# Optimization experiments

Hardware: AMD Instinct MI355X
Metric: run time of the kernel (lower is better)

Reference implementation:

```python
import jax, jax.numpy as jnp
import numpy as np

C_S, C_V, C_Z, C_OUT = 32, 8, 128, 128
IN_S, IN_V = 28, 37
N_RBF, N_POS = 64, 64
IN_Z = N_RBF * 25 + N_POS          # 1664 raw pairwise-dist RBF + positional feats
N_LAYERS, K = 4, 30
N_NODES = 1024
N_EDGES = N_NODES * K
WEIGHT_NUMEL = C_S*C_S + C_S*C_V + C_V*C_V + C_V*C_S + C_V*C_V  # 1664
LN_EPS = 1e-5
BN_EPS = 1e-5


def _ln(x, g, b):
    m = x.mean(-1, keepdims=True)
    v = x.var(-1, keepdims=True)
    return (x - m) / jnp.sqrt(v + LN_EPS) * g + b


def _tp(xs, xv, sh_s, sh_v, w):
    """FullyConnectedTensorProduct (32x0e+8x1e) x (0e+1e) -> (32x0e+8x1e), per-edge weights w [E, WEIGHT_NUMEL]."""
    E = w.shape[0]
    o = [0]
    def cut(n1, n2):
        ww = w[:, o[0]:o[0] + n1 * n2].reshape(E, n1, n2)
        o[0] += n1 * n2
        return ww
    w1 = cut(C_S, C_S)  # 0e x 0e -> 0e
    w2 = cut(C_S, C_V)  # 0e x 1e -> 1e
    w3 = cut(C_V, C_V)  # 1e x 0e -> 1e
    w4 = cut(C_V, C_S)  # 1e x 1e -> 0e (dot)
    w5 = cut(C_V, C_V)  # 1e x 1e -> 1e (cross)
    # path normalization: 1/sqrt(in1_mul * n_paths_to_output)
    a1 = 1.0 / np.sqrt(2 * C_S)
    a4 = 1.0 / np.sqrt(2 * C_V)
    a2 = 1.0 / np.sqrt(3 * C_S)
    a3 = 1.0 / np.sqrt(3 * C_V)
    a5 = a3
    out_s = a1 * jnp.einsum('e,ei,eij->ej', sh_s, xs, w1) \
          + (a4 / np.sqrt(3.0)) * jnp.einsum('eix,ex,eij->ej', xv, sh_v, w4)
    cross = jnp.cross(xv, sh_v[:, None, :])  # [E, C_V, 3]
    out_v = a2 * jnp.einsum('ei,eij,ex->ejx', xs, w2, sh_v) \
          + a3 * jnp.einsum('e,eix,eij->ejx', sh_s, xv, w3) \
          + (a5 / np.sqrt(2.0)) * jnp.einsum('eix,eij->ejx', cross, w5)
    return out_s, out_v


def _forward(node_raw, edge_raw, edge_vecs, rot,
             ee_w1, ee_b1, ee_w2, ee_b2, ee_w3, ee_b3, ee_ln_g, ee_ln_b,
             ne_ws, ne_wv,
             fc_w1, fc_b1, fc_w2, fc_b2, bn_g, bn_b, bn_vg,
             eu_lin, eu_w1, eu_b1, eu_w2, eu_b2, eu_w3, eu_b3, eu_ln_g, eu_ln_b,
             mu_w, mu_b, lv_w, lv_b, edge_index):
    N = node_raw.shape[0]
    dst, src = edge_index[0], edge_index[1]
    # spherical harmonics, lmax=1, 'component' normalization: Y0 = 1, Y1 = sqrt(3) * unit
    unit = edge_vecs / (jnp.linalg.norm(edge_vecs, axis=-1, keepdims=True) + 1e-8)
    sh_s = jnp.ones(edge_vecs.shape[0], node_raw.dtype)
    sh_v = np.sqrt(3.0) * unit
    # edge embed MLP + LN
    h = jax.nn.relu(edge_raw @ ee_w1 + ee_b1)
    h = jax.nn.relu(h @ ee_w2 + ee_b2)
    ef = _ln(h @ ee_w3 + ee_b3, ee_ln_g, ee_ln_b)
    # node embed: per-irrep (equivariant) linear 28x0e->32x0e, 37x1e->8x1e
    xs = node_raw[:, :IN_S] @ ne_ws
    xv = jnp.einsum('nix,ij->njx', node_raw[:, IN_S:].reshape(N, IN_V, 3), ne_wv)
    cnt = jnp.maximum(jax.ops.segment_sum(jnp.ones_like(src, node_raw.dtype), src, num_segments=N), 1.0)
    for l in range(N_LAYERS):
        # per-edge TP weights from edge features
        w = jax.nn.relu(ef @ fc_w1[l] + fc_b1[l]) @ fc_w2[l] + fc_b2[l]  # [E, WEIGHT_NUMEL]
        ms, mv = _tp(xs[dst], xv[dst], sh_s, sh_v, w)
        ags = jax.ops.segment_sum(ms, src, num_segments=N) / cnt[:, None]
        agv = jax.ops.segment_sum(mv, src, num_segments=N) / cnt[:, None, None]
        xs = xs + ags  # pad is a no-op: in/out irreps identical
        xv = xv + agv
        # e3nn-style BatchNorm (batch statistics)
        xs = (xs - xs.mean(0)) / jnp.sqrt(xs.var(0) + BN_EPS) * bn_g[l] + bn_b[l]
        fn = jnp.mean(jnp.sum(xv ** 2, -1), 0) / 3.0  # per-channel mean component norm
        xv = xv / jnp.sqrt(fn + BN_EPS)[None, :, None] * bn_vg[l][None, :, None]
        # EdgeUpdate
        a = xs @ eu_lin[l]  # scalar part -> h_edge
        e_in = jnp.concatenate([a[dst], a[src], ef], -1)
        u = jax.nn.relu(e_in @ eu_w1[l] + eu_b1[l])
        u = jax.nn.relu(u @ eu_w2[l] + eu_b2[l])
        u = u @ eu_w3[l] + eu_b3[l]
        ef = _ln(ef + u, eu_ln_g[l], eu_ln_b[l])
    # scalarize vectors w.r.t. per-node frames: R^T v
    xv_loc = jnp.einsum('nxy,ncx->ncy', rot, xv)
    feat = jnp.concatenate([xs, xv_loc.reshape(N, -1)], -1)  # [N, 56]
    mu = feat @ mu_w + mu_b
    lv = feat @ lv_w + lv_b
    return jnp.stack([mu, lv])  # [2, N, C_OUT]


def setup_inputs() -> dict:
    key = jax.random.key(0)
    ks = iter(jax.random.split(key, 80))
    def nrm(shape, fan=None):
        s = 1.0 if fan is None else 1.0 / np.sqrt(fan)
        return jax.random.normal(next(ks), shape, jnp.float32) * s
    inp = {}
    inp['node_raw'] = nrm([N_NODES, IN_S + 3 * IN_V])
    inp['edge_raw'] = nrm([N_EDGES, IN_Z])
    inp['edge_vecs'] = nrm([N_EDGES, 3])
    inp['rot'] = jnp.linalg.qr(nrm([N_NODES, 3, 3]))[0]
    inp['edge_index'] = jax.random.randint(next(ks), (2, N_EDGES), 0, N_NODES, jnp.int32)
    inp['ee_w1'] = nrm([IN_Z, C_Z], IN_Z); inp['ee_b1'] = jnp.zeros([C_Z])
    inp['ee_w2'] = nrm([C_Z, C_Z], C_Z);   inp['ee_b2'] = jnp.zeros([C_Z])
    inp['ee_w3'] = nrm([C_Z, C_Z], C_Z);   inp['ee_b3'] = jnp.zeros([C_Z])
    inp['ee_ln_g'] = jnp.ones([C_Z]); inp['ee_ln_b'] = jnp.zeros([C_Z])
    inp['ne_ws'] = nrm([IN_S, C_S], IN_S)
    inp['ne_wv'] = nrm([IN_V, C_V], IN_V)
    L = N_LAYERS
    inp['fc_w1'] = nrm([L, C_Z, C_Z], C_Z); inp['fc_b1'] = jnp.zeros([L, C_Z])
    inp['fc_w2'] = nrm([L, C_Z, WEIGHT_NUMEL], C_Z); inp['fc_b2'] = jnp.zeros([L, WEIGHT_NUMEL])
    inp['bn_g'] = jnp.ones([L, C_S]); inp['bn_b'] = jnp.zeros([L, C_S]); inp['bn_vg'] = jnp.ones([L, C_V])
    inp['eu_lin'] = nrm([L, C_S, C_Z], C_S)
    inp['eu_w1'] = nrm([L, 3 * C_Z, C_Z], 3 * C_Z); inp['eu_b1'] = jnp.zeros([L, C_Z])
    inp['eu_w2'] = nrm([L, C_Z, C_Z], C_Z); inp['eu_b2'] = jnp.zeros([L, C_Z])
    inp['eu_w3'] = nrm([L, C_Z, C_Z], C_Z); inp['eu_b3'] = jnp.zeros([L, C_Z])
    inp['eu_ln_g'] = jnp.ones([L, C_Z]); inp['eu_ln_b'] = jnp.zeros([L, C_Z])
    D = C_S + 3 * C_V
    inp['mu_w'] = nrm([D, C_OUT], D); inp['mu_b'] = jnp.zeros([C_OUT])
    inp['lv_w'] = nrm([D, C_OUT], D); inp['lv_b'] = jnp.zeros([C_OUT])
    return inp


def reference(node_raw, edge_raw, edge_vecs, rot,
              ee_w1, ee_b1, ee_w2, ee_b2, ee_w3, ee_b3, ee_ln_g, ee_ln_b,
              ne_ws, ne_wv,
              fc_w1, fc_b1, fc_w2, fc_b2, bn_g, bn_b, bn_vg,
              eu_lin, eu_w1, eu_b1, eu_w2, eu_b2, eu_w3, eu_b3, eu_ln_g, eu_ln_b,
              mu_w, mu_b, lv_w, lv_b, edge_index):
    return _forward(node_raw, edge_raw, edge_vecs, rot,
                    ee_w1, ee_b1, ee_w2, ee_b2, ee_w3, ee_b3, ee_ln_g, ee_ln_b,
                    ne_ws, ne_wv,
                    fc_w1, fc_b1, fc_w2, fc_b2, bn_g, bn_b, bn_vg,
                    eu_lin, eu_w1, eu_b1, eu_w2, eu_b2, eu_w3, eu_b3, eu_ln_g, eu_ln_b,
                    mu_w, mu_b, lv_w, lv_b, edge_index)
```

## Files before the change

### kernel.cpp

```cpp
#include <hip/hip_runtime.h>
#include <hip/hip_bf16.h>

typedef __hip_bfloat16 bf16;
typedef __attribute__((ext_vector_type(8))) short s16x8;
typedef __attribute__((ext_vector_type(4))) float f32x4;

#define NN 1024
#define NE 30720
#define CS 32
#define CV 8
#define CZ 128
#define INS 28
#define INV 37
#define NRDIM 139
#define INZ 1664
#define WN 1664
#define NL 4

__device__ __forceinline__ float b2f(bf16 x) { return __bfloat162float(x); }
__device__ __forceinline__ bf16 f2b(float x) { return __float2bfloat16(x); }


template<int RELU, int AF32, int GATHER>
__global__ __launch_bounds__(256)
void gemm64(const void* __restrict__ Ap, const bf16* __restrict__ Bf,
            const float* __restrict__ bias, bf16* __restrict__ Cp,
            int M, int K,
            const bf16* __restrict__ g_a, const bf16* __restrict__ g_ef,
            const int* __restrict__ g_ei)
{
    __shared__ __align__(16) bf16 la[64 * 40];
    const int bm = blockIdx.x * 64;
    const int tid = threadIdx.x;
    const int lane = tid & 63;
    const int wv = tid >> 6;
    const int lr = tid >> 1;
    const int lc = (tid & 1) * 16;
    const int l15 = lane & 15;
    const int quad = lane >> 4;
    const int K32 = K >> 5;
    f32x4 acc[4][2] = {};
    const bf16*  ga16 = (const bf16*) Ap + (size_t)(bm + lr) * K + lc;
    const float* ga32 = (const float*)Ap + (size_t)(bm + lr) * K + lc;
    int gdst = 0, gsrc = 0, grow = 0;
    if (GATHER && tid < 128) {
        grow = bm + lr;
        gdst = g_ei[grow];
        gsrc = g_ei[NE + grow];
    }
    for (int k0 = 0; k0 < K; k0 += 32) {
        union { bf16 h[16]; float4 q[2]; } pa;
        if (tid < 128) {
            if (AF32) {
                float4 f0 = *(const float4*)(ga32 + k0);
                float4 f1 = *(const float4*)(ga32 + k0 + 4);
                float4 f2 = *(const float4*)(ga32 + k0 + 8);
                float4 f3 = *(const float4*)(ga32 + k0 + 12);
                pa.h[0]=f2b(f0.x); pa.h[1]=f2b(f0.y); pa.h[2]=f2b(f0.z); pa.h[3]=f2b(f0.w);
                pa.h[4]=f2b(f1.x); pa.h[5]=f2b(f1.y); pa.h[6]=f2b(f1.z); pa.h[7]=f2b(f1.w);
                pa.h[8]=f2b(f2.x); pa.h[9]=f2b(f2.y); pa.h[10]=f2b(f2.z); pa.h[11]=f2b(f2.w);
                pa.h[12]=f2b(f3.x); pa.h[13]=f2b(f3.y); pa.h[14]=f2b(f3.z); pa.h[15]=f2b(f3.w);
            } else if (GATHER) {
                int kk = k0 + lc;
                const bf16* src;
                if (kk < 128)      src = g_a  + (size_t)gdst * CZ + kk;
                else if (kk < 256) src = g_a  + (size_t)gsrc * CZ + (kk - 128);
                else               src = g_ef + (size_t)grow * CZ + (kk - 256);
                pa.q[0] = *(const float4*)src;
                pa.q[1] = *(const float4*)(src + 8);
            } else {
                pa.q[0] = *(const float4*)(ga16 + k0);
                pa.q[1] = *(const float4*)(ga16 + k0 + 8);
            }
        }
        s16x8 bfr[2];
#pragma unroll
        for (int ni = 0; ni < 2; ni++)
            bfr[ni] = *(const s16x8*)(Bf + (size_t)(((wv * 2 + ni) * K32 + (k0 >> 5)) * 512) + lane * 8);
        __syncthreads();
        if (tid < 128) {
            *(float4*)&la[lr * 40 + lc]     = pa.q[0];
            *(float4*)&la[lr * 40 + lc + 8] = pa.q[1];
        }
        __syncthreads();
        s16x8 af[4];
#pragma unroll
        for (int mi = 0; mi < 4; mi++)
            af[mi] = *(const s16x8*)&la[(mi * 16 + l15) * 40 + quad * 8];
#pragma unroll
        for (int mi = 0; mi < 4; mi++)
#pragma unroll
            for (int ni = 0; ni < 2; ni++)
                acc[mi][ni] = __builtin_amdgcn_mfma_f32_16x16x32_bf16(af[mi], bfr[ni], acc[mi][ni], 0, 0, 0);
    }
#pragma unroll
    for (int ni = 0; ni < 2; ni++) {
        const int col = wv * 32 + ni * 16 + l15;
        const float bv = bias[col];
#pragma unroll
        for (int mi = 0; mi < 4; mi++) {
            const int row0 = bm + mi * 16 + quad * 4;
#pragma unroll
            for (int r = 0; r < 4; r++) {
                float v = acc[mi][ni][r] + bv;
                if (RELU) v = fmaxf(v, 0.f);
                Cp[(size_t)(row0 + r) * CZ + col] = f2b(v);
            }
        }
    }
}

template<int RESID>
__global__ __launch_bounds__(256)
void mlp2(const bf16* __restrict__ A,
          const bf16* __restrict__ w2f, const float* __restrict__ b2,
          const bf16* __restrict__ w3f, const float* __restrict__ b3,
          const float* __restrict__ g, const float* __restrict__ bb,
          bf16* efb)
{
    __shared__ __align__(16) bf16 s_a[64 * 136];
    __shared__ __align__(16) bf16 s_u[64 * 136];
    __shared__ float s_o[64 * 132];
    const int bm = blockIdx.x * 64;
    const int t = threadIdx.x;
    const int lane = t & 63;
    const int wv = t >> 6;
    const int l15 = lane & 15;
    const int quad = lane >> 4;
    {
        int r = t >> 2, c0 = (t & 3) * 32;
        const float4* s4 = (const float4*)(A + (size_t)(bm + r) * CZ + c0);
        float4* d4 = (float4*)&s_a[r * 136 + c0];
        d4[0] = s4[0]; d4[1] = s4[1]; d4[2] = s4[2]; d4[3] = s4[3];
    }
    __syncthreads();
    s16x8 af[4][4];
#pragma unroll
    for (int mi = 0; mi < 4; mi++)
#pragma unroll
        for (int kk = 0; kk < 4; kk++)
            af[mi][kk] = *(const s16x8*)&s_a[(mi * 16 + l15) * 136 + kk * 32 + quad * 8];
#pragma unroll
    for (int s = 0; s < 2; s++) {
        int n = wv * 32 + s * 16 + l15;
        f32x4 acc[4] = {};
#pragma unroll
        for (int kk = 0; kk < 4; kk++) {
            s16x8 bfr = *(const s16x8*)(w2f + (size_t)(((wv * 2 + s) * 4 + kk) * 512) + lane * 8);
#pragma unroll
            for (int mi = 0; mi < 4; mi++)
                acc[mi] = __builtin_amdgcn_mfma_f32_16x16x32_bf16(af[mi][kk], bfr, acc[mi], 0, 0, 0);
        }
        float bv = b2[n];
#pragma unroll
        for (int mi = 0; mi < 4; mi++)
#pragma unroll
            for (int r = 0; r < 4; r++)
                s_u[(mi * 16 + quad * 4 + r) * 136 + n] = f2b(fmaxf(acc[mi][r] + bv, 0.f));
    }
    __syncthreads();
#pragma unroll
    for (int mi = 0; mi < 4; mi++)
#pragma unroll
        for (int kk = 0; kk < 4; kk++)
            af[mi][kk] = *(const s16x8*)&s_u[(mi * 16 + l15) * 136 + kk * 32 + quad * 8];
#pragma unroll
    for (int s = 0; s < 2; s++) {
        int n = wv * 32 + s * 16 + l15;
        f32x4 acc[4] = {};
#pragma unroll
        for (int kk = 0; kk < 4; kk++) {
            s16x8 bfr = *(const s16x8*)(w3f + (size_t)(((wv * 2 + s) * 4 + kk) * 512) + lane * 8);
#pragma unroll
            for (int mi = 0; mi < 4; mi++)
                acc[mi] = __builtin_amdgcn_mfma_f32_16x16x32_bf16(af[mi][kk], bfr, acc[mi], 0, 0, 0);
        }
        float bv = b3[n];
#pragma unroll
        for (int mi = 0; mi < 4; mi++)
#pragma unroll
            for (int r = 0; r < 4; r++)
                s_o[(mi * 16 + quad * 4 + r) * 132 + n] = acc[mi][r] + bv;
    }
    __syncthreads();
    {
        int row = wv * 16 + (lane >> 2);
        int q = lane & 3;
        int col0 = q * 32;
        size_t gbase = (size_t)(bm + row) * CZ;
        float s = 0.f, s2 = 0.f;
        for (int i = 0; i < 32; i++) {
            float x = s_o[row * 132 + col0 + i];
            if (RESID) x += b2f(efb[gbase + col0 + i]);
            s += x; s2 += x * x;
        }
        s  += __shfl_xor(s, 1);  s2 += __shfl_xor(s2, 1);
        s  += __shfl_xor(s, 2);  s2 += __shfl_xor(s2, 2);
        float mean = s * (1.f / 128.f);
        float var  = s2 * (1.f / 128.f) - mean * mean;
        float rstd = rsqrtf(var + 1e-5f);
        for (int i = 0; i < 32; i++) {
            int col = col0 + i;
            float x = s_o[row * 132 + col];
            if (RESID) x += b2f(efb[gbase + col]);
            efb[gbase + col] = f2b((x - mean) * rstd * g[col] + bb[col]);
        }
    }
}

__global__ __launch_bounds__(256, 2)
void fc2_tp(const bf16* __restrict__ ef,
            const bf16* __restrict__ w1f, const float* __restrict__ b1,
            const bf16* __restrict__ w2f, const float* __restrict__ b2,
            const int* __restrict__ ei, const float* __restrict__ edge_vecs,
            const float* __restrict__ xs, const float* __restrict__ xv,
            float* __restrict__ tp_s, float* __restrict__ tp_v)
{
    __shared__ __align__(16) bf16 s_a[64 * 136];
    __shared__ __align__(16) bf16 s_h[64 * 136];
    __shared__ __align__(16) float s_xsT[32][64];
    __shared__ __align__(16) float s_xvT[24][64];
    __shared__ __align__(16) float s_crT[24][64];
    __shared__ __align__(16) float s_y4T[8][64];
    __shared__ __align__(16) float s_b2[WN];
    __shared__ float s_shv[64][3];
    __shared__ int s_dst[64];
    __shared__ float s_os[64][32];
    __shared__ float s_ov[64][24];
    const int be = blockIdx.x * 64;
    const int t = threadIdx.x;
    const int lane = t & 63;
    const int wv = t >> 6;
    const int l15 = lane & 15;
    const int quad = lane >> 4;
    const int q4 = quad * 4;

    if (t < 64) {
        int e = be + t;
        s_dst[t] = ei[e];
        float vx = edge_vecs[e * 3 + 0];
        float vy = edge_vecs[e * 3 + 1];
        float vz = edge_vecs[e * 3 + 2];
        float sc = 1.7320508075688772f / (sqrtf(vx * vx + vy * vy + vz * vz) + 1e-8f);
        s_shv[t][0] = vx * sc; s_shv[t][1] = vy * sc; s_shv[t][2] = vz * sc;
    }
    for (int i = t; i < 64 * 32; i += 256) ((float*)s_os)[i] = 0.f;
    for (int i = t; i < 64 * 24; i += 256) ((float*)s_ov)[i] = 0.f;
    for (int i = t; i < WN; i += 256) s_b2[i] = b2[i];
    {
        int r = t >> 2, c0 = (t & 3) * 32;
        const float4* s4 = (const float4*)(ef + (size_t)(be + r) * CZ + c0);
        float4* d4 = (float4*)&s_a[r * 136 + c0];
        d4[0] = s4[0]; d4[1] = s4[1]; d4[2] = s4[2]; d4[3] = s4[3];
    }
    __syncthreads();
    for (int i = t; i < 64 * 32; i += 256) { int e = i & 63, c = i >> 6; s_xsT[c][e] = xs[s_dst[e] * CS + c]; }
    for (int i = t; i < 64 * 24; i += 256) { int e = i & 63, c = i >> 6; s_xvT[c][e] = xv[s_dst[e] * 24 + c]; }
    __syncthreads();
    for (int i2 = t; i2 < 512; i2 += 256) {
        int e = i2 & 63, i = i2 >> 6;
        float h0 = s_shv[e][0], h1 = s_shv[e][1], h2 = s_shv[e][2];
        float x0 = s_xvT[i * 3 + 0][e], x1 = s_xvT[i * 3 + 1][e], x2 = s_xvT[i * 3 + 2][e];
        s_y4T[i][e] = 1.1547005383792515f * (x0 * h0 + x1 * h1 + x2 * h2);
        s_crT[i * 3 + 0][e] = 0.7071067811865476f * (x1 * h2 - x2 * h1);
        s_crT[i * 3 + 1][e] = 0.7071067811865476f * (x2 * h0 - x0 * h2);
        s_crT[i * 3 + 2][e] = 0.7071067811865476f * (x0 * h1 - x1 * h0);
    }
    {
        s16x8 af1[4][4];
#pragma unroll
        for (int mi = 0; mi < 4; mi++)
#pragma unroll
            for (int kk = 0; kk < 4; kk++)
                af1[mi][kk] = *(const s16x8*)&s_a[(mi * 16 + l15) * 136 + kk * 32 + quad * 8];
#pragma unroll
        for (int s = 0; s < 2; s++) {
            int n = wv * 32 + s * 16 + l15;
            f32x4 acc[4] = {};
#pragma unroll
            for (int kk = 0; kk < 4; kk++) {
                s16x8 bfr = *(const s16x8*)(w1f + (size_t)(((wv * 2 + s) * 4 + kk) * 512) + lane * 8);
#pragma unroll
                for (int mi = 0; mi < 4; mi++)
                    acc[mi] = __builtin_amdgcn_mfma_f32_16x16x32_bf16(af1[mi][kk], bfr, acc[mi], 0, 0, 0);
            }
            float bv = b1[n];
#pragma unroll
            for (int mi = 0; mi < 4; mi++)
#pragma unroll
                for (int r = 0; r < 4; r++)
                    s_h[(mi * 16 + quad * 4 + r) * 136 + n] = f2b(fmaxf(acc[mi][r] + bv, 0.f));
        }
    }
    __syncthreads();
    s16x8 af[4][4];
#pragma unroll
    for (int mi = 0; mi < 4; mi++)
#pragma unroll
        for (int kk = 0; kk < 4; kk++)
            af[mi][kk] = *(const s16x8*)&s_h[(mi * 16 + l15) * 136 + kk * 32 + quad * 8];
    float os[4][4] = {}, sv2[4][4] = {}, ov0[4][4] = {}, ov1[4][4] = {}, ov2[4][4] = {};
    const int ib = l15 >> 3;
    for (int nt = wv; nt < 104; nt += 4) {
        const float bv = s_b2[nt * 16 + l15];
        const bf16* wb = w2f + (size_t)(nt * 4) * 512 + lane * 8;
        s16x8 bfr[4];
#pragma unroll
        for (int kk = 0; kk < 4; kk++)
            bfr[kk] = *(const s16x8*)(wb + kk * 512);
        f32x4 ac[4] = {};
#pragma unroll
        for (int kk = 0; kk < 4; kk++)
#pragma unroll
            for (int mi = 0; mi < 4; mi++)
                ac[mi] = __builtin_amdgcn_mfma_f32_16x16x32_bf16(af[mi][kk], bfr[kk], ac[mi], 0, 0, 0);
        if (nt < 64) {
            const int i = nt >> 1;
#pragma unroll
            for (int mi = 0; mi < 4; mi++) {
                float4 f = *(const float4*)&s_xsT[i][mi * 16 + q4];
                os[mi][0] += (ac[mi][0] + bv) * f.x; os[mi][1] += (ac[mi][1] + bv) * f.y;
                os[mi][2] += (ac[mi][2] + bv) * f.z; os[mi][3] += (ac[mi][3] + bv) * f.w;
            }
        } else if (nt < 80) {
            const int i = (nt - 64) * 2 + ib;
#pragma unroll
            for (int mi = 0; mi < 4; mi++) {
                float4 f = *(const float4*)&s_xsT[i][mi * 16 + q4];
                sv2[mi][0] += (ac[mi][0] + bv) * f.x; sv2[mi][1] += (ac[mi][1] + bv) * f.y;
                sv2[mi][2] += (ac[mi][2] + bv) * f.z; sv2[mi][3] += (ac[mi][3] + bv) * f.w;
            }
        } else if (nt < 84) {
            const int i0 = ((nt - 80) * 2 + ib) * 3;
#pragma unroll
            for (int mi = 0; mi < 4; mi++) {
                float4 f0 = *(const float4*)&s_xvT[i0 + 0][mi * 16 + q4];
                float4 f1 = *(const float4*)&s_xvT[i0 + 1][mi * 16 + q4];
                float4 f2 = *(const float4*)&s_xvT[i0 + 2][mi * 16 + q4];
                float w0 = ac[mi][0] + bv, w1 = ac[mi][1] + bv, w2 = ac[mi][2] + bv, w3 = ac[mi][3] + bv;
                ov0[mi][0] += w0 * f0.x; ov0[mi][1] += w1 * f0.y; ov0[mi][2] += w2 * f0.z; ov0[mi][3] += w3 * f0.w;
                ov1[mi][0] += w0 * f1.x; ov1[mi][1] += w1 * f1.y; ov1[mi][2] += w2 * f1.z; ov1[mi][3] += w3 * f1.w;
                ov2[mi][0] += w0 * f2.x; ov2[mi][1] += w1 * f2.y; ov2[mi][2] += w2 * f2.z; ov2[mi][3] += w3 * f2.w;
            }
        } else if (nt < 100) {
            const int i = (nt - 84) >> 1;
#pragma unroll
            for (int mi = 0; mi < 4; mi++) {
                float4 f = *(const float4*)&s_y4T[i][mi * 16 + q4];
                os[mi][0] += (ac[mi][0] + bv) * f.x; os[mi][1] += (ac[mi][1] + bv) * f.y;
                os[mi][2] += (ac[mi][2] + bv) * f.z; os[mi][3] += (ac[mi][3] + bv) * f.w;
            }
        } else {
            const int i0 = ((nt - 100) * 2 + ib) * 3;
#pragma unroll
            for (int mi = 0; mi < 4; mi++) {
                float4 f0 = *(const float4*)&s_crT[i0 + 0][mi * 16 + q4];
                float4 f1 = *(const float4*)&s_crT[i0 + 1][mi * 16 + q4];
                float4 f2 = *(const float4*)&s_crT[i0 + 2][mi * 16 + q4];
                float w0 = ac[mi][0] + bv, w1 = ac[mi][1] + bv, w2 = ac[mi][2] + bv, w3 = ac[mi][3] + bv;
                ov0[mi][0] += w0 * f0.x; ov0[mi][1] += w1 * f0.y; ov0[mi][2] += w2 * f0.z; ov0[mi][3] += w3 * f0.w;
                ov1[mi][0] += w0 * f1.x; ov1[mi][1] += w1 * f1.y; ov1[mi][2] += w2 * f1.z; ov1[mi][3] += w3 * f1.w;
                ov2[mi][0] += w0 * f2.x; ov2[mi][1] += w1 * f2.y; ov2[mi][2] += w2 * f2.z; ov2[mi][3] += w3 * f2.w;
            }
        }
    }
    {
        const int jo = (wv & 1) * 16 + l15;
        const int jv3 = (l15 & 7) * 3;
#pragma unroll
        for (int mi = 0; mi < 4; mi++)
#pragma unroll
            for (int r = 0; r < 4; r++) {
                int e = mi * 16 + quad * 4 + r;
                atomicAdd(&s_os[e][jo], os[mi][r]);
                float sv = 0.5f * sv2[mi][r];
                atomicAdd(&s_ov[e][jv3 + 0], ov0[mi][r] + s_shv[e][0] * sv);
                atomicAdd(&s_ov[e][jv3 + 1], ov1[mi][r] + s_shv[e][1] * sv);
                atomicAdd(&s_ov[e][jv3 + 2], ov2[mi][r] + s_shv[e][2] * sv);
            }
    }
    __syncthreads();
    for (int i = t; i < 64 * 32; i += 256) {
        int e = i >> 5, d = i & 31;
        tp_s[(size_t)(be + e) * 32 + d] = s_os[e][d] * 0.125f;
    }
    for (int i = t; i < 64 * 24; i += 256) {
        int e = i / 24, d = i - e * 24;
        tp_v[(size_t)(be + e) * 24 + d] = s_ov[e][d] * 0.2041241452319315f;
    }
}

__global__ __launch_bounds__(1024)
void scan_csr(const int* __restrict__ cnt, int* __restrict__ row_start,
              int* __restrict__ fillpos, float* __restrict__ icnt)
{
    __shared__ int tmp[1024];
    int t = threadIdx.x;
    int v = cnt[t];
    tmp[t] = v;
    __syncthreads();
    for (int o = 1; o < 1024; o <<= 1) {
        int x = (t >= o) ? tmp[t - o] : 0;
        __syncthreads();
        tmp[t] += x;
        __syncthreads();
    }
    int excl = tmp[t] - v;
    row_start[t] = excl;
    fillpos[t] = excl;
    if (t == 1023) row_start[1024] = tmp[1023];
    icnt[t] = 1.0f / (float)(v > 1 ? v : 1);
}

__global__ void fill_perm(const int* __restrict__ ei, int* __restrict__ fillpos,
                          int* __restrict__ perm)
{
    int e = blockIdx.x * 256 + threadIdx.x;
    if (e < NE) {
        int s = ei[NE + e];
        int p = atomicAdd(&fillpos[s], 1);
        perm[p] = e;
    }
}

__global__ __launch_bounds__(64)
void aggregate(const float* __restrict__ tp_s, const float* __restrict__ tp_v,
               const int* __restrict__ perm, const int* __restrict__ row_start,
               const float* __restrict__ icnt,
               float* __restrict__ ags, float* __restrict__ agv)
{
    __shared__ int s_e[64];
    const int n = blockIdx.x, t = threadIdx.x;
    const int s = row_start[n], epe = row_start[n + 1];
    float acc = 0.f;
    for (int k0 = s; k0 < epe; k0 += 64) {
        int kk = k0 + t;
        s_e[t] = (kk < epe) ? perm[kk] : 0;
        __syncthreads();
        int m = epe - k0; if (m > 64) m = 64;
        for (int j = 0; j < m; j++) {
            int e = s_e[j];
            acc += (t < 32) ? tp_s[(size_t)e * 32 + t]
                            : tp_v[(size_t)e * 24 + (t - 32)];
        }
        __syncthreads();
    }
    acc *= icnt[n];
    if (t < 32) ags[n * CS + t] = acc;
    else if (t < 56) agv[n * 24 + (t - 32)] = acc;
}

__device__ __forceinline__ void fragseg(int i, int R, int C,
                                        const float* __restrict__ s, bf16* __restrict__ d)
{
    int l = i / (R * C);
    int rem = i - l * R * C;
    int k = rem / C;
    int n = rem - k * C;
    int dst = ((n >> 4) * (R >> 5) + (k >> 5)) * 512 + ((k >> 3) & 3) * 128 + (n & 15) * 8 + (k & 7);
    d[(size_t)l * R * C + dst] = f2b(s[i]);
}

__global__ void transpose_all(const float* __restrict__ p0, const float* __restrict__ p1,
                              const float* __restrict__ p2, const float* __restrict__ p3,
                              const float* __restrict__ p4, const float* __restrict__ p5,
                              const float* __restrict__ p6, const float* __restrict__ p7,
                              bf16* d0, bf16* d1, bf16* d2, bf16* d3,
                              bf16* d4, bf16* d5, bf16* d6, bf16* d7)
{
    int i = blockIdx.x * 256 + threadIdx.x;
    const int S0 = INZ * CZ;
    const int S1 = CZ * CZ;
    const int S2 = CZ * CZ;
    const int S3 = NL * CZ * CZ;
    const int S4 = NL * CZ * WN;
    const int S5 = NL * 384 * CZ;
    const int S6 = NL * CZ * CZ;
    const int S7 = NL * CZ * CZ;
    if (i < S0) { fragseg(i, INZ, CZ, p0, d0); return; } i -= S0;
    if (i < S1) { fragseg(i, CZ, CZ, p1, d1); return; }  i -= S1;
    if (i < S2) { fragseg(i, CZ, CZ, p2, d2); return; }  i -= S2;
    if (i < S3) { fragseg(i, CZ, CZ, p3, d3); return; }  i -= S3;
    if (i < S4) { fragseg(i, CZ, WN, p4, d4); return; }  i -= S4;
    if (i < S5) { fragseg(i, 384, CZ, p5, d5); return; } i -= S5;
    if (i < S6) { fragseg(i, CZ, CZ, p6, d6); return; }  i -= S6;
    if (i < S7) { fragseg(i, CZ, CZ, p7, d7); return; }
}

__global__ __launch_bounds__(64)
void node_embed(const float* __restrict__ node_raw, const float* __restrict__ ne_ws,
                const float* __restrict__ ne_wv, float* __restrict__ xs, float* __restrict__ xv)
{
    int n = blockIdx.x, t = threadIdx.x;
    const float* nr = node_raw + (size_t)n * NRDIM;
    if (t < 32) {
        float acc = 0.f;
        for (int i = 0; i < INS; i++) acc += nr[i] * ne_ws[i * CS + t];
        xs[n * CS + t] = acc;
    } else if (t < 56) {
        int t2 = t - 32, j = t2 / 3, x = t2 - 3 * (t2 / 3);
        float acc = 0.f;
        for (int i = 0; i < INV; i++) acc += nr[INS + i * 3 + x] * ne_wv[i * CV + j];
        xv[n * 24 + t2] = acc;
    }
}

__global__ void count_src(const int* __restrict__ ei, int* __restrict__ cnt)
{
    int e = blockIdx.x * 256 + threadIdx.x;
    if (e < NE) atomicAdd(&cnt[ei[NE + e]], 1);
}

__global__ __launch_bounds__(256)
void bnfused(float* __restrict__ xs, float* __restrict__ xv,
             const float* __restrict__ ags, const float* __restrict__ agv,
             const float* __restrict__ g, const float* __restrict__ b,
             const float* __restrict__ vg)
{
    __shared__ float red[8];
    __shared__ float stat[2];
    int c = blockIdx.x, t = threadIdx.x;
    if (c < 32) {
        float s = 0.f, s2 = 0.f;
        for (int n = t; n < NN; n += 256) {
            float v = xs[n * CS + c] + ags[n * CS + c];
            s += v; s2 += v * v;
        }
        for (int o = 32; o > 0; o >>= 1) { s += __shfl_down(s, o); s2 += __shfl_down(s2, o); }
        int w = t >> 6;
        if ((t & 63) == 0) { red[w * 2] = s; red[w * 2 + 1] = s2; }
        __syncthreads();
        if (t == 0) {
            float S = red[0] + red[2] + red[4] + red[6];
            float S2 = red[1] + red[3] + red[5] + red[7];
            float mean = S * (1.f / NN);
            float var = S2 * (1.f / NN) - mean * mean;
            stat[0] = mean;
            stat[1] = rsqrtf(var + 1e-5f);
        }
        __syncthreads();
        float mean = stat[0], rstd = stat[1], gg = g[c], bb = b[c];
        for (int n = t; n < NN; n += 256) {
            int ix = n * CS + c;
            float v = xs[ix] + ags[ix];
            xs[ix] = (v - mean) * rstd * gg + bb;
        }
    } else {
        int c2 = c - 32;
        float s = 0.f;
        for (int n = t; n < NN; n += 256) {
            float v0 = xv[n * 24 + c2 * 3 + 0] + agv[n * 24 + c2 * 3 + 0];
            float v1 = xv[n * 24 + c2 * 3 + 1] + agv[n * 24 + c2 * 3 + 1];
            float v2 = xv[n * 24 + c2 * 3 + 2] + agv[n * 24 + c2 * 3 + 2];
            s += v0 * v0 + v1 * v1 + v2 * v2;
        }
        for (int o = 32; o > 0; o >>= 1) s += __shfl_down(s, o);
        int w = t >> 6;
        if ((t & 63) == 0) red[w] = s;
        __syncthreads();
        if (t == 0) {
            float fn = (red[0] + red[1] + red[2] + red[3]) * (1.f / (3.f * NN));
            stat[0] = vg[c2] * rsqrtf(fn + 1e-5f);
        }
        __syncthreads();
        float scale = stat[0];
        for (int n = t; n < NN; n += 256) {
            for (int x = 0; x < 3; x++) {
                int ix = n * 24 + c2 * 3 + x;
                xv[ix] = (xv[ix] + agv[ix]) * scale;
            }
        }
    }
}

__global__ __launch_bounds__(128)
void lin_a(const float* __restrict__ xs, const float* __restrict__ eu_lin_l,
           bf16* __restrict__ a_b)
{
    __shared__ float sxs[32];
    int n = blockIdx.x, t = threadIdx.x;
    if (t < 32) sxs[t] = xs[n * CS + t];
    __syncthreads();
    float acc = 0.f;
    for (int c = 0; c < 32; c++) acc += sxs[c] * eu_lin_l[c * CZ + t];
    a_b[(size_t)n * CZ + t] = f2b(acc);
}

__global__ __launch_bounds__(128)
void final_out(const float* __restrict__ xs, const float* __restrict__ xv,
               const float* __restrict__ rot,
               const float* __restrict__ mu_w, const float* __restrict__ mu_b,
               const float* __restrict__ lv_w, const float* __restrict__ lv_b,
               float* __restrict__ out)
{
    __shared__ float feat[56];
    int n = blockIdx.x, t = threadIdx.x;
    if (t < 32) feat[t] = xs[n * CS + t];
    else if (t < 56) {
        int t2 = t - 32, c = t2 / 3, y = t2 - 3 * (t2 / 3);
        float acc = 0.f;
        for (int x = 0; x < 3; x++)
            acc += rot[n * 9 + x * 3 + y] * xv[n * 24 + c * 3 + x];
        feat[t] = acc;
    }
    __syncthreads();
    float mu = mu_b[t], lv = lv_b[t];
    for (int d = 0; d < 56; d++) {
        float f = feat[d];
        mu += f * mu_w[d * 128 + t];
        lv += f * lv_w[d * 128 + t];
    }
    out[(size_t)n * 128 + t] = mu;
    out[(size_t)NN * 128 + (size_t)n * 128 + t] = lv;
}

extern "C" void kernel_launch(void* const* d_in, const int* in_sizes, int n_in,
                              void* d_out, int out_size, void* d_ws, size_t ws_size,
                              hipStream_t stream)
{
    (void)in_sizes; (void)n_in; (void)out_size; (void)ws_size;
    const float* node_raw  = (const float*)d_in[0];
    const float* edge_raw  = (const float*)d_in[1];
    const float* edge_vecs = (const float*)d_in[2];
    const float* rot       = (const float*)d_in[3];
    const int*   ei        = (const int*  )d_in[4];
    const float* ee_w1 = (const float*)d_in[5];
    const float* ee_b1 = (const float*)d_in[6];
    const float* ee_w2 = (const float*)d_in[7];
    const float* ee_b2 = (const float*)d_in[8];
    const float* ee_w3 = (const float*)d_in[9];
    const float* ee_b3 = (const float*)d_in[10];
    const float* ee_ln_g = (const float*)d_in[11];
    const float* ee_ln_b = (const float*)d_in[12];
    const float* ne_ws = (const float*)d_in[13];
    const float* ne_wv = (const float*)d_in[14];
    const float* fc_w1 = (const float*)d_in[15];
    const float* fc_b1 = (const float*)d_in[16];
    const float* fc_w2 = (const float*)d_in[17];
    const float* fc_b2 = (const float*)d_in[18];
    const float* bn_g  = (const float*)d_in[19];
    const float* bn_b  = (const float*)d_in[20];
    const float* bn_vg = (const float*)d_in[21];
    const float* eu_lin = (const float*)d_in[22];
    const float* eu_w1 = (const float*)d_in[23];
    const float* eu_b1 = (const float*)d_in[24];
    const float* eu_w2 = (const float*)d_in[25];
    const float* eu_b2 = (const float*)d_in[26];
    const float* eu_w3 = (const float*)d_in[27];
    const float* eu_b3 = (const float*)d_in[28];
    const float* eu_ln_g = (const float*)d_in[29];
    const float* eu_ln_b = (const float*)d_in[30];
    const float* mu_w = (const float*)d_in[31];
    const float* mu_b = (const float*)d_in[32];
    const float* lv_w = (const float*)d_in[33];
    const float* lv_b = (const float*)d_in[34];

    char* ws = (char*)d_ws;
    size_t off = 0;
    auto alloc = [&](size_t bytes) -> void* {
        void* p = ws + off;
        off += (bytes + 255) & ~(size_t)255;
        return p;
    };
    bf16*  ef_b  = (bf16*) alloc((size_t)NE * CZ * 2);
    bf16*  buf_a = (bf16*) alloc((size_t)NE * CZ * 2);
    float* xs    = (float*)alloc((size_t)NN * CS * 4);
    float* xv    = (float*)alloc((size_t)NN * 24 * 4);
    float* ags   = (float*)alloc((size_t)NN * CS * 4);
    float* agv   = (float*)alloc((size_t)NN * 24 * 4);
    int*   cnti  = (int*)  alloc((size_t)NN * 4);
    float* icnt  = (float*)alloc((size_t)NN * 4);
    bf16*  a_b   = (bf16*) alloc((size_t)NN * CZ * 2);
    float* tp_s  = (float*)alloc((size_t)NE * 32 * 4);
    float* tp_v  = (float*)alloc((size_t)NE * 24 * 4 + 64);
    int*   perm  = (int*)  alloc((size_t)NE * 4);
    int*   row_start = (int*)alloc((size_t)(NN + 1) * 4);
    int*   fillpos   = (int*)alloc((size_t)NN * 4);
    bf16* ee_w1t = (bf16*)alloc((size_t)INZ * CZ * 2);
    bf16* ee_w2t = (bf16*)alloc((size_t)CZ * CZ * 2);
    bf16* ee_w3t = (bf16*)alloc((size_t)CZ * CZ * 2);
    bf16* fc_w1t = (bf16*)alloc((size_t)NL * CZ * CZ * 2);
    bf16* fc_w2t = (bf16*)alloc((size_t)NL * WN * CZ * 2);
    bf16* eu_w1t = (bf16*)alloc((size_t)NL * 384 * CZ * 2);
    bf16* eu_w2t = (bf16*)alloc((size_t)NL * CZ * CZ * 2);
    bf16* eu_w3t = (bf16*)alloc((size_t)NL * CZ * CZ * 2);

    const int TRN = INZ*CZ + 2*CZ*CZ + NL*CZ*CZ + NL*CZ*WN + NL*384*CZ + 2*NL*CZ*CZ;
    transpose_all<<<(TRN + 255) / 256, 256, 0, stream>>>(
        ee_w1, ee_w2, ee_w3, fc_w1, fc_w2, eu_w1, eu_w2, eu_w3,
        ee_w1t, ee_w2t, ee_w3t, fc_w1t, fc_w2t, eu_w1t, eu_w2t, eu_w3t);

    node_embed<<<NN, 64, 0, stream>>>(node_raw, ne_ws, ne_wv, xs, xv);
    hipMemsetAsync(cnti, 0, NN * 4, stream);
    count_src<<<NE / 256, 256, 0, stream>>>(ei, cnti);
    scan_csr<<<1, 1024, 0, stream>>>(cnti, row_start, fillpos, icnt);
    fill_perm<<<NE / 256, 256, 0, stream>>>(ei, fillpos, perm);

    const int GE = NE / 64;
    gemm64<1, 1, 0><<<GE, 256, 0, stream>>>(edge_raw, ee_w1t, ee_b1, buf_a, NE, INZ, nullptr, nullptr, nullptr);
    mlp2<0><<<GE, 256, 0, stream>>>(buf_a, ee_w2t, ee_b2, ee_w3t, ee_b3, ee_ln_g, ee_ln_b, ef_b);

    for (int l = 0; l < NL; l++) {
        fc2_tp<<<NE / 64, 256, 0, stream>>>(
            ef_b, fc_w1t + (size_t)l * CZ * CZ, fc_b1 + l * CZ,
            fc_w2t + (size_t)l * WN * CZ, fc_b2 + l * WN,
            ei, edge_vecs, xs, xv, tp_s, tp_v);
        aggregate<<<NN, 64, 0, stream>>>(tp_s, tp_v, perm, row_start, icnt, ags, agv);
        bnfused<<<40, 256, 0, stream>>>(xs, xv, ags, agv,
                                        bn_g + l * CS, bn_b + l * CS, bn_vg + l * CV);
        lin_a<<<NN, 128, 0, stream>>>(xs, eu_lin + (size_t)l * CS * CZ, a_b);
        gemm64<1, 0, 1><<<GE, 256, 0, stream>>>(
            nullptr, eu_w1t + (size_t)l * 384 * CZ, eu_b1 + l * CZ, buf_a, NE, 384, a_b, ef_b, ei);
        mlp2<1><<<GE, 256, 0, stream>>>(buf_a, eu_w2t + (size_t)l * CZ * CZ, eu_b2 + l * CZ,
                                        eu_w3t + (size_t)l * CZ * CZ, eu_b3 + l * CZ,
                                        eu_ln_g + l * CZ, eu_ln_b + l * CZ, ef_b);
    }

    final_out<<<NN, 128, 0, stream>>>(xs, xv, rot, mu_w, mu_b, lv_w, lv_b, (float*)d_out);
}
```

Measured before the change: 946.6 us.

## Fold node linear into edge-update W1 and fuse edge-update MLP into one kernel

Precomputes eu_lin·W1 products for the dst and src blocks so each node's contribution to the first edge-update layer is a per-node 128-wide vector, replacing a 384-K gathered GEMM with a 128-K GEMM plus a gathered add. The whole edge-update MLP (three layers, residual and layer norm) is fused into one kernel, so the intermediate activation no longer round-trips through global memory. In exchange it adds a small fold kernel, per-node fp32 projection buffers, and a change in rounding because the node terms are no longer quantized to bf16 before the matmul.

Measured after the change: 877.4 us. -7.3%, faster.

```diff
diff --git a/kernel.cpp b/kernel.cpp
--- a/kernel.cpp
+++ b/kernel.cpp
@@ -21,13 +21,11 @@
 __device__ __forceinline__ bf16 f2b(float x) { return __float2bfloat16(x); }
 
 
-template<int RELU, int AF32, int GATHER>
+template<int RELU, int AF32>
 __global__ __launch_bounds__(256)
 void gemm64(const void* __restrict__ Ap, const bf16* __restrict__ Bf,
             const float* __restrict__ bias, bf16* __restrict__ Cp,
-            int M, int K,
-            const bf16* __restrict__ g_a, const bf16* __restrict__ g_ef,
-            const int* __restrict__ g_ei)
+            int M, int K)
 {
     __shared__ __align__(16) bf16 la[64 * 40];
     const int bm = blockIdx.x * 64;
@@ -42,12 +40,6 @@
     f32x4 acc[4][2] = {};
     const bf16*  ga16 = (const bf16*) Ap + (size_t)(bm + lr) * K + lc;
     const float* ga32 = (const float*)Ap + (size_t)(bm + lr) * K + lc;
-    int gdst = 0, gsrc = 0, grow = 0;
-    if (GATHER && tid < 128) {
-        grow = bm + lr;
-        gdst = g_ei[grow];
-        gsrc = g_ei[NE + grow];
-    }
     for (int k0 = 0; k0 < K; k0 += 32) {
         union { bf16 h[16]; float4 q[2]; } pa;
         if (tid < 128) {
@@ -60,14 +52,6 @@
                 pa.h[4]=f2b(f1.x); pa.h[5]=f2b(f1.y); pa.h[6]=f2b(f1.z); pa.h[7]=f2b(f1.w);
                 pa.h[8]=f2b(f2.x); pa.h[9]=f2b(f2.y); pa.h[10]=f2b(f2.z); pa.h[11]=f2b(f2.w);
                 pa.h[12]=f2b(f3.x); pa.h[13]=f2b(f3.y); pa.h[14]=f2b(f3.z); pa.h[15]=f2b(f3.w);
-            } else if (GATHER) {
-                int kk = k0 + lc;
-                const bf16* src;
-                if (kk < 128)      src = g_a  + (size_t)gdst * CZ + kk;
-                else if (kk < 256) src = g_a  + (size_t)gsrc * CZ + (kk - 128);
-                else               src = g_ef + (size_t)grow * CZ + (kk - 256);
-                pa.q[0] = *(const float4*)src;
-                pa.q[1] = *(const float4*)(src + 8);
             } else {
                 pa.q[0] = *(const float4*)(ga16 + k0);
                 pa.q[1] = *(const float4*)(ga16 + k0 + 8);
@@ -110,7 +94,6 @@
     }
 }
 
-template<int RESID>
 __global__ __launch_bounds__(256)
 void mlp2(const bf16* __restrict__ A,
           const bf16* __restrict__ w2f, const float* __restrict__ b2,
@@ -191,7 +174,6 @@
         float s = 0.f, s2 = 0.f;
         for (int i = 0; i < 32; i++) {
             float x = s_o[row * 132 + col0 + i];
-            if (RESID) x += b2f(efb[gbase + col0 + i]);
             s += x; s2 += x * x;
         }
         s  += __shfl_xor(s, 1);  s2 += __shfl_xor(s2, 1);
@@ -202,7 +184,150 @@
         for (int i = 0; i < 32; i++) {
             int col = col0 + i;
             float x = s_o[row * 132 + col];
-            if (RESID) x += b2f(efb[gbase + col]);
+            efb[gbase + col] = f2b((x - mean) * rstd * g[col] + bb[col]);
+        }
+    }
+}
+
+__global__ __launch_bounds__(256)
+void eu_fused(bf16* __restrict__ efb,
+              const float* __restrict__ adg, const float* __restrict__ asg,
+              const int* __restrict__ ei,
+              const bf16* __restrict__ w1cf, const float* __restrict__ b1,
+              const bf16* __restrict__ w2f, const float* __restrict__ b2,
+              const bf16* __restrict__ w3f, const float* __restrict__ b3,
+              const float* __restrict__ g, const float* __restrict__ bb)
+{
+    __shared__ __align__(16) bf16 s_a[64 * 136];
+    __shared__ __align__(16) bf16 s_u1[64 * 136];
+    __shared__ __align__(16) float s_go[64 * 132];
+    bf16* const s_u2 = (bf16*)s_go;
+    const int bm = blockIdx.x * 64;
+    const int t = threadIdx.x;
+    const int lane = t & 63;
+    const int wv = t >> 6;
+    const int l15 = lane & 15;
+    const int quad = lane >> 4;
+    {
+        int r = t >> 2, c0 = (t & 3) * 32;
+        const float4* s4 = (const float4*)(efb + (size_t)(bm + r) * CZ + c0);
+        float4* d4 = (float4*)&s_a[r * 136 + c0];
+        d4[0] = s4[0]; d4[1] = s4[1]; d4[2] = s4[2]; d4[3] = s4[3];
+        int dst = ei[bm + r], src = ei[NE + bm + r];
+        const float4* pd = (const float4*)(adg + (size_t)dst * CZ + c0);
+        const float4* ps = (const float4*)(asg + (size_t)src * CZ + c0);
+        float4* dg = (float4*)&s_go[r * 132 + c0];
+#pragma unroll
+        for (int k = 0; k < 8; k++) {
+            float4 va = pd[k], vb = ps[k];
+            dg[k] = make_float4(va.x + vb.x, va.y + vb.y, va.z + vb.z, va.w + vb.w);
+        }
+    }
+    __syncthreads();
+    {
+        s16x8 af[4][4];
+#pragma unroll
+        for (int mi = 0; mi < 4; mi++)
+#pragma unroll
+            for (int kk = 0; kk < 4; kk++)
+                af[mi][kk] = *(const s16x8*)&s_a[(mi * 16 + l15) * 136 + kk * 32 + quad * 8];
+#pragma unroll
+        for (int s = 0; s < 2; s++) {
+            int n = wv * 32 + s * 16 + l15;
+            f32x4 acc[4] = {};
+#pragma unroll
+            for (int kk = 0; kk < 4; kk++) {
+                s16x8 bfr = *(const s16x8*)(w1cf + (size_t)(((wv * 2 + s) * 4 + kk) * 512) + lane * 8);
+#pragma unroll
+                for (int mi = 0; mi < 4; mi++)
+                    acc[mi] = __builtin_amdgcn_mfma_f32_16x16x32_bf16(af[mi][kk], bfr, acc[mi], 0, 0, 0);
+            }
+            float bv = b1[n];
+#pragma unroll
+            for (int mi = 0; mi < 4; mi++)
+#pragma unroll
+                for (int r = 0; r < 4; r++) {
+                    int e = mi * 16 + quad * 4 + r;
+                    s_u1[e * 136 + n] = f2b(fmaxf(acc[mi][r] + bv + s_go[e * 132 + n], 0.f));
+                }
+        }
+    }
+    __syncthreads();
+    {
+        s16x8 af[4][4];
+#pragma unroll
+        for (int mi = 0; mi < 4; mi++)
+#pragma unroll
+            for (int kk = 0; kk < 4; kk++)
+                af[mi][kk] = *(const s16x8*)&s_u1[(mi * 16 + l15) * 136 + kk * 32 + quad * 8];
+#pragma unroll
+        for (int s = 0; s < 2; s++) {
+            int n = wv * 32 + s * 16 + l15;
+            f32x4 acc[4] = {};
+#pragma unroll
+            for (int kk = 0; kk < 4; kk++) {
+                s16x8 bfr = *(const s16x8*)(w2f + (size_t)(((wv * 2 + s) * 4 + kk) * 512) + lane * 8);
+#pragma unroll
+                for (int mi = 0; mi < 4; mi++)
+                    acc[mi] = __builtin_amdgcn_mfma_f32_16x16x32_bf16(af[mi][kk], bfr, acc[mi], 0, 0, 0);
+            }
+            float bv = b2[n];
+#pragma unroll
+            for (int mi = 0; mi < 4; mi++)
+#pragma unroll
+                for (int r = 0; r < 4; r++)
+                    s_u2[(mi * 16 + quad * 4 + r) * 136 + n] = f2b(fmaxf(acc[mi][r] + bv, 0.f));
+        }
+    }
+    __syncthreads();
+    {
+        s16x8 af[4][4];
+#pragma unroll
+        for (int mi = 0; mi < 4; mi++)
+#pragma unroll
+            for (int kk = 0; kk < 4; kk++)
+                af[mi][kk] = *(const s16x8*)&s_u2[(mi * 16 + l15) * 136 + kk * 32 + quad * 8];
+        __syncthreads();
+#pragma unroll
+        for (int s = 0; s < 2; s++) {
+            int n = wv * 32 + s * 16 + l15;
+            f32x4 acc[4] = {};
+#pragma unroll
+            for (int kk = 0; kk < 4; kk++) {
+                s16x8 bfr = *(const s16x8*)(w3f + (size_t)(((wv * 2 + s) * 4 + kk) * 512) + lane * 8);
+#pragma unroll
+                for (int mi = 0; mi < 4; mi++)
+                    acc[mi] = __builtin_amdgcn_mfma_f32_16x16x32_bf16(af[mi][kk], bfr, acc[mi], 0, 0, 0);
+            }
+            float bv = b3[n];
+#pragma unroll
+            for (int mi = 0; mi < 4; mi++)
+#pragma unroll
+                for (int r = 0; r < 4; r++) {
+                    int e = mi * 16 + quad * 4 + r;
+                    s_go[e * 132 + n] = acc[mi][r] + bv + b2f(s_a[e * 136 + n]);
+                }
+        }
+    }
+    __syncthreads();
+    {
+        int row = wv * 16 + (lane >> 2);
+        int q = lane & 3;
+        int col0 = q * 32;
+        size_t gbase = (size_t)(bm + row) * CZ;
+        float s = 0.f, s2 = 0.f;
+        for (int i = 0; i < 32; i++) {
+            float x = s_go[row * 132 + col0 + i];
+            s += x; s2 += x * x;
+        }
+        s  += __shfl_xor(s, 1);  s2 += __shfl_xor(s2, 1);
+        s  += __shfl_xor(s, 2);  s2 += __shfl_xor(s2, 2);
+        float mean = s * (1.f / 128.f);
+        float var  = s2 * (1.f / 128.f) - mean * mean;
+        float rstd = rsqrtf(var + 1e-5f);
+        for (int i = 0; i < 32; i++) {
+            int col = col0 + i;
+            float x = s_go[row * 132 + col];
             efb[gbase + col] = f2b((x - mean) * rstd * g[col] + bb[col]);
         }
     }
@@ -482,9 +607,55 @@
     if (i < S2) { fragseg(i, CZ, CZ, p2, d2); return; }  i -= S2;
     if (i < S3) { fragseg(i, CZ, CZ, p3, d3); return; }  i -= S3;
     if (i < S4) { fragseg(i, CZ, WN, p4, d4); return; }  i -= S4;
-    if (i < S5) { fragseg(i, 384, CZ, p5, d5); return; } i -= S5;
+    if (i < S5) {
+        int l = i / (384 * CZ);
+        int rem = i - l * (384 * CZ);
+        int k = rem / CZ, n = rem - k * CZ;
+        if (k >= 256) {
+            int k2 = k - 256;
+            int dst = ((n >> 4) * (CZ >> 5) + (k2 >> 5)) * 512 + ((k2 >> 3) & 3) * 128 + (n & 15) * 8 + (k2 & 7);
+            d5[(size_t)l * CZ * CZ + dst] = f2b(p5[i]);
+        }
+        return;
+    } i -= S5;
     if (i < S6) { fragseg(i, CZ, CZ, p6, d6); return; }  i -= S6;
     if (i < S7) { fragseg(i, CZ, CZ, p7, d7); return; }
+}
+
+__global__ __launch_bounds__(256)
+void fold_f(const float* __restrict__ eu_lin, const float* __restrict__ eu_w1,
+            float* __restrict__ Fw)
+{
+    int b = blockIdx.x, t = threadIdx.x;
+    int l = b >> 1, part = b & 1;
+    const float* L = eu_lin + (size_t)l * CS * CZ;
+    const float* W = eu_w1 + (size_t)l * 384 * CZ + (size_t)part * CZ * CZ;
+    float* out = Fw + (size_t)b * CS * CZ;
+    for (int idx = t; idx < CS * CZ; idx += 256) {
+        int i = idx >> 7, n = idx & 127;
+        float acc = 0.f;
+        for (int k = 0; k < CZ; k++)
+            acc += L[i * CZ + k] * W[k * CZ + n];
+        out[idx] = acc;
+    }
+}
+
+__global__ __launch_bounds__(128)
+void adas(const float* __restrict__ xs, const float* __restrict__ Fd,
+          const float* __restrict__ Fs, float* __restrict__ adg, float* __restrict__ asg)
+{
+    __shared__ float sxs[32];
+    int n = blockIdx.x, t = threadIdx.x;
+    if (t < 32) sxs[t] = xs[n * CS + t];
+    __syncthreads();
+    float a = 0.f, b = 0.f;
+    for (int i = 0; i < 32; i++) {
+        float x = sxs[i];
+        a += x * Fd[i * CZ + t];
+        b += x * Fs[i * CZ + t];
+    }
+    adg[(size_t)n * CZ + t] = a;
+    asg[(size_t)n * CZ + t] = b;
 }
 
 __global__ __launch_bounds__(64)
@@ -571,19 +742,6 @@
             }
         }
     }
-}
-
-__global__ __launch_bounds__(128)
-void lin_a(const float* __restrict__ xs, const float* __restrict__ eu_lin_l,
-           bf16* __restrict__ a_b)
-{
-    __shared__ float sxs[32];
-    int n = blockIdx.x, t = threadIdx.x;
-    if (t < 32) sxs[t] = xs[n * CS + t];
-    __syncthreads();
-    float acc = 0.f;
-    for (int c = 0; c < 32; c++) acc += sxs[c] * eu_lin_l[c * CZ + t];
-    a_b[(size_t)n * CZ + t] = f2b(acc);
 }
 
 __global__ __launch_bounds__(128)
@@ -670,7 +828,9 @@
     float* agv   = (float*)alloc((size_t)NN * 24 * 4);
     int*   cnti  = (int*)  alloc((size_t)NN * 4);
     float* icnt  = (float*)alloc((size_t)NN * 4);
-    bf16*  a_b   = (bf16*) alloc((size_t)NN * CZ * 2);
+    float* adg   = (float*)alloc((size_t)NN * CZ * 4);
+    float* asg   = (float*)alloc((size_t)NN * CZ * 4);
+    float* Fw    = (float*)alloc((size_t)NL * 2 * CS * CZ * 4);
     float* tp_s  = (float*)alloc((size_t)NE * 32 * 4);
     float* tp_v  = (float*)alloc((size_t)NE * 24 * 4 + 64);
     int*   perm  = (int*)  alloc((size_t)NE * 4);
@@ -681,14 +841,15 @@
     bf16* ee_w3t = (bf16*)alloc((size_t)CZ * CZ * 2);
     bf16* fc_w1t = (bf16*)alloc((size_t)NL * CZ * CZ * 2);
     bf16* fc_w2t = (bf16*)alloc((size_t)NL * WN * CZ * 2);
-    bf16* eu_w1t = (bf16*)alloc((size_t)NL * 384 * CZ * 2);
+    bf16* eu_w1ct = (bf16*)alloc((size_t)NL * CZ * CZ * 2);
     bf16* eu_w2t = (bf16*)alloc((size_t)NL * CZ * CZ * 2);
     bf16* eu_w3t = (bf16*)alloc((size_t)NL * CZ * CZ * 2);
 
     const int TRN = INZ*CZ + 2*CZ*CZ + NL*CZ*CZ + NL*CZ*WN + NL*384*CZ + 2*NL*CZ*CZ;
     transpose_all<<<(TRN + 255) / 256, 256, 0, stream>>>(
         ee_w1, ee_w2, ee_w3, fc_w1, fc_w2, eu_w1, eu_w2, eu_w3,
-        ee_w1t, ee_w2t, ee_w3t, fc_w1t, fc_w2t, eu_w1t, eu_w2t, eu_w3t);
+        ee_w1t, ee_w2t, ee_w3t, fc_w1t, fc_w2t, eu_w1ct, eu_w2t, eu_w3t);
+    fold_f<<<NL * 2, 256, 0, stream>>>(eu_lin, eu_w1, Fw);
 
     node_embed<<<NN, 64, 0, stream>>>(node_raw, ne_ws, ne_wv, xs, xv);
     hipMemsetAsync(cnti, 0, NN * 4, stream);
@@ -697,23 +858,25 @@
     fill_perm<<<NE / 256, 256, 0, stream>>>(ei, fillpos, perm);
 
     const int GE = NE / 64;
-    gemm64<1, 1, 0><<<GE, 256, 0, stream>>>(edge_raw, ee_w1t, ee_b1, buf_a, NE, INZ, nullptr, nullptr, nullptr);
-    mlp2<0><<<GE, 256, 0, stream>>>(buf_a, ee_w2t, ee_b2, ee_w3t, ee_b3, ee_ln_g, ee_ln_b, ef_b);
+    gemm64<1, 1><<<GE, 256, 0, stream>>>(edge_raw, ee_w1t, ee_b1, buf_a, NE, INZ);
+    mlp2<<<GE, 256, 0, stream>>>(buf_a, ee_w2t, ee_b2, ee_w3t, ee_b3, ee_ln_g, ee_ln_b, ef_b);
 
     for (int l = 0; l < NL; l++) {
-        fc2_tp<<<NE / 64, 256, 0, stream>>>(
+        fc2_tp<<<GE, 256, 0, stream>>>(
             ef_b, fc_w1t + (size_t)l * CZ * CZ, fc_b1 + l * CZ,
             fc_w2t + (size_t)l * WN * CZ, fc_b2 + l * WN,
             ei, edge_vecs, xs, xv, tp_s, tp_v);
         aggregate<<<NN, 64, 0, stream>>>(tp_s, tp_v, perm, row_start, icnt, ags, agv);
         bnfused<<<40, 256, 0, stream>>>(xs, xv, ags, agv,
                                         bn_g + l * CS, bn_b + l * CS, bn_vg + l * CV);
-        lin_a<<<NN, 128, 0, stream>>>(xs, eu_lin + (size_t)l * CS * CZ, a_b);
-        gemm64<1, 0, 1><<<GE, 256, 0, stream>>>(
-            nullptr, eu_w1t + (size_t)l * 384 * CZ, eu_b1 + l * CZ, buf_a, NE, 384, a_b, ef_b, ei);
-        mlp2<1><<<GE, 256, 0, stream>>>(buf_a, eu_w2t + (size_t)l * CZ * CZ, eu_b2 + l * CZ,
-                                        eu_w3t + (size_t)l * CZ * CZ, eu_b3 + l * CZ,
-                                        eu_ln_g + l * CZ, eu_ln_b + l * CZ, ef_b);
+        adas<<<NN, 128, 0, stream>>>(xs, Fw + (size_t)(l * 2) * CS * CZ,
+                                     Fw + (size_t)(l * 2 + 1) * CS * CZ, adg, asg);
+        eu_fused<<<GE, 256, 0, stream>>>(
+            ef_b, adg, asg, ei,
+            eu_w1ct + (size_t)l * CZ * CZ, eu_b1 + l * CZ,
+            eu_w2t + (size_t)l * CZ * CZ, eu_b2 + l * CZ,
+            eu_w3t + (size_t)l * CZ * CZ, eu_b3 + l * CZ,
+            eu_ln_g + l * CZ, eu_ln_b + l * CZ);
     }
 
     final_out<<<NN, 128, 0, stream>>>(xs, xv, rot, mu_w, mu_b, lv_w, lv_b, (float*)d_out);
```
